# Performance work log

Hardware: AMD Instinct MI355X
Metric: run time of the kernel (lower is better)

The kernel has to match this reference:

```python
import jax, jax.numpy as jnp
import numpy as np

# Segmented tensor-product configuration (matches init_kwargs)
NUM_SEG = 32   # segments per operand
MUL = 128      # multiplicity ('u' axis) of operand0 / output segments
D = 3          # irrep dimension (2l+1 with l=1) for i, j, k axes
NUM_PATHS = 64
BATCH = 2048


def setup_inputs() -> dict:
    key = jax.random.key(0)
    k0, k1, k2, k3, k4, k5 = jax.random.split(key, 6)
    x0 = jax.random.normal(k0, (BATCH, NUM_SEG * MUL * D), dtype=jnp.float32)
    x1 = jax.random.normal(k1, (BATCH, NUM_SEG * D), dtype=jnp.float32)
    coeff = jax.random.normal(k2, (NUM_PATHS, D, D, D), dtype=jnp.float32)
    idx0 = jax.random.randint(k3, (NUM_PATHS,), 0, NUM_SEG, dtype=jnp.int32)
    idx1 = jax.random.randint(k4, (NUM_PATHS,), 0, NUM_SEG, dtype=jnp.int32)
    idx2 = jax.random.randint(k5, (NUM_PATHS,), 0, NUM_SEG, dtype=jnp.int32)
    return {"x0": x0, "x1": x1, "coeff": coeff,
            "idx0": idx0, "idx1": idx1, "idx2": idx2}


def reference(x0, x1, coeff, idx0, idx1, idx2):
    # Segmented CG tensor product:
    #   out[seg2][u,k] += sum_{paths p with idx2[p]==seg2}
    #       sum_ij x0[idx0[p]][u,i] * x1[idx1[p]][j] * coeff[p][i,j,k]
    B = x0.shape[0]
    x0s = x0.reshape(B, NUM_SEG, MUL, D)   # 'ui' segments
    x1s = x1.reshape(B, NUM_SEG, D)        # 'j' segments
    # gather input segments per path
    x0p = x0s[:, idx0]                     # (B, P, MUL, D)
    x1p = x1s[:, idx1]                     # (B, P, D)
    # per-path contraction with path coefficients, path axis first for scatter
    contrib = jnp.einsum('bpui,bpj,pijk->pbuk', x0p, x1p, coeff)
    # scatter-add contributions into output segments
    out_seg = jax.ops.segment_sum(contrib, idx2, num_segments=NUM_SEG)  # (S, B, MUL, D)
    out = jnp.transpose(out_seg, (1, 0, 2, 3)).reshape(B, NUM_SEG * MUL * D)
    return out
```

## Files before the change

kernel.cpp:

```cpp
#include <hip/hip_runtime.h>

#define NUM_SEG 32
#define MUL 128
#define D 3
#define NUM_PATHS 64
#define ROW (NUM_SEG * MUL * D)
#define SEGF (MUL * D)
#define HALF_F4 1536
#define SEG_HF 192

typedef float v2f __attribute__((ext_vector_type(2)));
typedef float v4f __attribute__((ext_vector_type(4)));

__global__ __launch_bounds__(256) void ftp_kernel(
    const float* __restrict__ x0, const float* __restrict__ x1,
    const float* __restrict__ coeff, const int* __restrict__ idx0,
    const int* __restrict__ idx1, const int* __restrict__ idx2,
    float* __restrict__ out)
{
    const int bid = blockIdx.x;
    const int b   = bid >> 1;
    const int h   = bid & 1;
    const int tid = threadIdx.x;

    __shared__ v4f   s_x0[HALF_F4];
    __shared__ float s_m[NUM_PATHS][9];
    __shared__ unsigned short s_pe[NUM_SEG][NUM_PATHS];
    __shared__ int   s_cnt[NUM_SEG];

    if (tid < NUM_SEG) s_cnt[tid] = 0;
    __syncthreads();

    const v4f* __restrict__ src = (const v4f*)(x0 + (size_t)b * ROW);
    #pragma unroll
    for (int j = 0; j < 6; ++j) {
        const int f     = j * 256 + tid;
        const int seg   = f / 48;
        const int inner = f - seg * 48;
        s_x0[f] = src[seg * 96 + h * 48 + inner];
    }

    if (tid < NUM_PATHS) {
        const int p  = tid;
        const int s0 = idx0[p];
        const int i1 = idx1[p];
        const int s2 = idx2[p];
        const int pos = atomicAdd(&s_cnt[s2], 1);
        s_pe[s2][pos] = (unsigned short)(s0 | (p << 8));

        const float* xr = x1 + (size_t)b * (NUM_SEG * D) + i1 * D;
        const float j0 = xr[0], j1 = xr[1], j2 = xr[2];
        const float* cf = coeff + p * 27;
        #pragma unroll
        for (int i = 0; i < D; ++i)
            #pragma unroll
            for (int k = 0; k < D; ++k)
                s_m[p][i * 3 + k] = j0 * cf[i * 9 + k]
                                  + j1 * cf[i * 9 + 3 + k]
                                  + j2 * cf[i * 9 + 6 + k];
    }
    __syncthreads();

    const int q  = tid & 31;
    const int ss = tid >> 5;
    float* __restrict__ ob = out + (size_t)b * ROW + h * SEG_HF + q * 6;
    const float* __restrict__ sx = (const float*)s_x0;

    #pragma unroll
    for (int si = 0; si < 4; ++si) {
        const int s = ss + si * 8;
        float a00 = 0, a01 = 0, a02 = 0, a10 = 0, a11 = 0, a12 = 0;
        const int n = s_cnt[s];
        for (int t = 0; t < n; ++t) {
            const int e = s_pe[s][t];
            const float* xs = sx + (e & 255) * SEG_HF + q * 6;
            const float u00 = xs[0], u01 = xs[1], u02 = xs[2];
            const float u10 = xs[3], u11 = xs[4], u12 = xs[5];
            const float* m = s_m[e >> 8];
            a00 += u00 * m[0] + u01 * m[3] + u02 * m[6];
            a01 += u00 * m[1] + u01 * m[4] + u02 * m[7];
            a02 += u00 * m[2] + u01 * m[5] + u02 * m[8];
            a10 += u10 * m[0] + u11 * m[3] + u12 * m[6];
            a11 += u10 * m[1] + u11 * m[4] + u12 * m[7];
            a12 += u10 * m[2] + u11 * m[5] + u12 * m[8];
        }
        float* o = ob + s * SEGF;
        v2f O0 = {a00, a01}, O1 = {a02, a10}, O2 = {a11, a12};
        *(v2f*)(o + 0) = O0;
        *(v2f*)(o + 2) = O1;
        *(v2f*)(o + 4) = O2;
    }
}

extern "C" void kernel_launch(void* const* d_in, const int* in_sizes, int n_in,
                              void* d_out, int out_size, void* d_ws, size_t ws_size,
                              hipStream_t stream) {
    const float* x0    = (const float*)d_in[0];
    const float* x1    = (const float*)d_in[1];
    const float* coeff = (const float*)d_in[2];
    const int*   idx0  = (const int*)d_in[3];
    const int*   idx1  = (const int*)d_in[4];
    const int*   idx2  = (const int*)d_in[5];
    float* out = (float*)d_out;

    const int B = in_sizes[0] / ROW;
    ftp_kernel<<<B * 2, 256, 0, stream>>>(x0, x1, coeff, idx0, idx1, idx2, out);
}
```

Measured before the change: 192.1 us.

## Split into setup and main kernels reading x0 directly from global memory

Adds a setup kernel that builds the per-segment path schedule once and precomputes the per-batch, per-path 3x3 contracted matrices into workspace. The main kernel then skips LDS staging of x0 and reads segments straight from global memory with 128-bit vector loads, each thread handling four u-rows and two output segments. The aim is to remove the per-block LDS fill, the syncthreads and the redundant schedule building. The cost is an extra kernel launch, a global round trip for the matrices, and repeated uncached gathers of x0 segments when several paths share the same source segment. The original kernel remains as a fallback when the workspace is too small.

```diff
diff --git a/kernel.cpp b/kernel.cpp
--- a/kernel.cpp
+++ b/kernel.cpp
@@ -6,11 +6,119 @@
 #define NUM_PATHS 64
 #define ROW (NUM_SEG * MUL * D)
 #define SEGF (MUL * D)
-#define HALF_F4 1536
 #define SEG_HF 192
+#define PE_STRIDE 64
+#define M_PAD 12
 
 typedef float v2f __attribute__((ext_vector_type(2)));
 typedef float v4f __attribute__((ext_vector_type(4)));
+
+__global__ __launch_bounds__(64) void ftp_setup(
+    const float* __restrict__ x1, const float* __restrict__ coeff,
+    const int* __restrict__ idx0, const int* __restrict__ idx1,
+    const int* __restrict__ idx2,
+    unsigned int* __restrict__ sched, float* __restrict__ m)
+{
+    const int tid = threadIdx.x;
+    if (blockIdx.x == 0) {
+        __shared__ int lcnt[NUM_SEG];
+        __shared__ unsigned int lpe[NUM_SEG][PE_STRIDE];
+        if (tid < NUM_SEG) lcnt[tid] = 0;
+        __syncthreads();
+        {
+            const int p   = tid;
+            const int s2  = idx2[p];
+            const int pos = atomicAdd(&lcnt[s2], 1);
+            lpe[s2][pos]  = (unsigned int)(idx0[p] | (p << 8));
+        }
+        __syncthreads();
+        if (tid < NUM_SEG) sched[tid] = (unsigned int)lcnt[tid];
+        for (int j = tid; j < NUM_SEG * PE_STRIDE; j += 64) {
+            const int s = j / PE_STRIDE, t = j % PE_STRIDE;
+            sched[NUM_SEG + j] = (t < lcnt[s]) ? lpe[s][t] : 0u;
+        }
+    } else {
+        const int b = blockIdx.x - 1;
+        const int p = tid;
+        const float* xr = x1 + (size_t)b * (NUM_SEG * D) + idx1[p] * D;
+        const float j0 = xr[0], j1 = xr[1], j2 = xr[2];
+        const float* cf = coeff + p * 27;
+        float mv[M_PAD];
+        #pragma unroll
+        for (int i = 0; i < D; ++i)
+            #pragma unroll
+            for (int k = 0; k < D; ++k)
+                mv[i * 3 + k] = j0 * cf[i * 9 + k]
+                              + j1 * cf[i * 9 + 3 + k]
+                              + j2 * cf[i * 9 + 6 + k];
+        mv[9] = 0.f; mv[10] = 0.f; mv[11] = 0.f;
+        float* mp = m + ((size_t)b * NUM_PATHS + p) * M_PAD;
+        *(v4f*)(mp)     = *(const v4f*)(mv);
+        *(v4f*)(mp + 4) = *(const v4f*)(mv + 4);
+        *(v4f*)(mp + 8) = *(const v4f*)(mv + 8);
+    }
+}
+
+__global__ __launch_bounds__(256) void ftp_main(
+    const float* __restrict__ x0, const unsigned int* __restrict__ sched,
+    const float* __restrict__ m, float* __restrict__ out)
+{
+    const int bid = blockIdx.x;
+    const int b   = bid >> 1;
+    const int h   = bid & 1;
+    const int tid = threadIdx.x;
+    const int qq  = tid & 15;
+    const int ss  = tid >> 4;
+
+    const float* __restrict__ xb = x0  + (size_t)b * ROW + h * SEG_HF + qq * 12;
+    float* __restrict__       ob = out + (size_t)b * ROW + h * SEG_HF + qq * 12;
+    const float* __restrict__ mb = m + (size_t)b * NUM_PATHS * M_PAD;
+    const unsigned int* __restrict__ pe = sched + NUM_SEG;
+
+    const int n0 = (int)sched[ss];
+    const int n1 = (int)sched[ss + 16];
+
+    #pragma unroll
+    for (int si = 0; si < 2; ++si) {
+        const int s = ss + si * 16;
+        const int n = si ? n1 : n0;
+        const unsigned int* __restrict__ pes = pe + s * PE_STRIDE;
+        float a00 = 0, a01 = 0, a02 = 0, a10 = 0, a11 = 0, a12 = 0;
+        float a20 = 0, a21 = 0, a22 = 0, a30 = 0, a31 = 0, a32 = 0;
+        for (int t = 0; t < n; ++t) {
+            const unsigned e = pes[t];
+            const float* xs = xb + (e & 255u) * SEGF;
+            const v4f X0 = *(const v4f*)(xs);
+            const v4f X1 = *(const v4f*)(xs + 4);
+            const v4f X2 = *(const v4f*)(xs + 8);
+            const float* mp = mb + (e >> 8) * M_PAD;
+            const v4f MA = *(const v4f*)(mp);
+            const v4f MB = *(const v4f*)(mp + 4);
+            const float m22 = mp[8];
+            a00 += X0.x * MA.x + X0.y * MA.w + X0.z * MB.z;
+            a01 += X0.x * MA.y + X0.y * MB.x + X0.z * MB.w;
+            a02 += X0.x * MA.z + X0.y * MB.y + X0.z * m22;
+            a10 += X0.w * MA.x + X1.x * MA.w + X1.y * MB.z;
+            a11 += X0.w * MA.y + X1.x * MB.x + X1.y * MB.w;
+            a12 += X0.w * MA.z + X1.x * MB.y + X1.y * m22;
+            a20 += X1.z * MA.x + X1.w * MA.w + X2.x * MB.z;
+            a21 += X1.z * MA.y + X1.w * MB.x + X2.x * MB.w;
+            a22 += X1.z * MA.z + X1.w * MB.y + X2.x * m22;
+            a30 += X2.y * MA.x + X2.z * MA.w + X2.w * MB.z;
+            a31 += X2.y * MA.y + X2.z * MB.x + X2.w * MB.w;
+            a32 += X2.y * MA.z + X2.z * MB.y + X2.w * m22;
+        }
+        float* o = ob + s * SEGF;
+        v4f O0 = {a00, a01, a02, a10};
+        v4f O1 = {a11, a12, a20, a21};
+        v4f O2 = {a22, a30, a31, a32};
+        *(v4f*)(o)     = O0;
+        *(v4f*)(o + 4) = O1;
+        *(v4f*)(o + 8) = O2;
+    }
+}
+
+#define HALF_F4 1536
 
 __global__ __launch_bounds__(256) void ftp_kernel(
     const float* __restrict__ x0, const float* __restrict__ x1,
@@ -76,13 +184,13 @@
             const float* xs = sx + (e & 255) * SEG_HF + q * 6;
             const float u00 = xs[0], u01 = xs[1], u02 = xs[2];
             const float u10 = xs[3], u11 = xs[4], u12 = xs[5];
-            const float* m = s_m[e >> 8];
-            a00 += u00 * m[0] + u01 * m[3] + u02 * m[6];
-            a01 += u00 * m[1] + u01 * m[4] + u02 * m[7];
-            a02 += u00 * m[2] + u01 * m[5] + u02 * m[8];
-            a10 += u10 * m[0] + u11 * m[3] + u12 * m[6];
-            a11 += u10 * m[1] + u11 * m[4] + u12 * m[7];
-            a12 += u10 * m[2] + u11 * m[5] + u12 * m[8];
+            const float* mm = s_m[e >> 8];
+            a00 += u00 * mm[0] + u01 * mm[3] + u02 * mm[6];
+            a01 += u00 * mm[1] + u01 * mm[4] + u02 * mm[7];
+            a02 += u00 * mm[2] + u01 * mm[5] + u02 * mm[8];
+            a10 += u10 * mm[0] + u11 * mm[3] + u12 * mm[6];
+            a11 += u10 * mm[1] + u11 * mm[4] + u12 * mm[7];
+            a12 += u10 * mm[2] + u11 * mm[5] + u12 * mm[8];
         }
         float* o = ob + s * SEGF;
         v2f O0 = {a00, a01}, O1 = {a02, a10}, O2 = {a11, a12};
@@ -104,5 +212,17 @@
     float* out = (float*)d_out;
 
     const int B = in_sizes[0] / ROW;
-    ftp_kernel<<<B * 2, 256, 0, stream>>>(x0, x1, coeff, idx0, idx1, idx2, out);
-}
+
+    const size_t schedBytes = (size_t)(NUM_SEG + NUM_SEG * PE_STRIDE) * sizeof(unsigned int);
+    const size_t schedPad   = (schedBytes + 255) & ~(size_t)255;
+    const size_t mBytes     = (size_t)B * NUM_PATHS * M_PAD * sizeof(float);
+
+    if (ws_size >= schedPad + mBytes) {
+        unsigned int* sched = (unsigned int*)d_ws;
+        float*        m     = (float*)((char*)d_ws + schedPad);
+        ftp_setup<<<B + 1, 64, 0, stream>>>(x1, coeff, idx0, idx1, idx2, sched, m);
+        ftp_main<<<B * 2, 256, 0, stream>>>(x0, sched, m, out);
+    } else {
+        ftp_kernel<<<B * 2, 256, 0, stream>>>(x0, x1, coeff, idx0, idx1, idx2, out);
+    }
+}
```

New measurement: 214.9 us. +11.9%, slower.

## Process full batch row per block with direct-to-LDS loads and sorted segment schedule

Applied to the files above, without the earlier changes.

Each block now handles a whole batch row instead of half of one. The full 48KB x0 row is staged into LDS with global_load_lds, so data goes straight to shared memory without passing through registers. Path entries are compacted with prefix offsets, and output segments are sorted by path count and dealt to waves in a snake order to balance the work. Block indices are swizzled across groups of eight. The larger LDS footprint lowers the number of resident blocks per CU, and the serial insertion sort on one thread adds a small setup cost.

```diff
diff --git a/kernel.cpp b/kernel.cpp
--- a/kernel.cpp
+++ b/kernel.cpp
@@ -6,8 +6,6 @@
 #define NUM_PATHS 64
 #define ROW (NUM_SEG * MUL * D)
 #define SEGF (MUL * D)
-#define HALF_F4 1536
-#define SEG_HF 192
 
 typedef float v2f __attribute__((ext_vector_type(2)));
 typedef float v4f __attribute__((ext_vector_type(4)));
@@ -16,73 +14,102 @@
     const float* __restrict__ x0, const float* __restrict__ x1,
     const float* __restrict__ coeff, const int* __restrict__ idx0,
     const int* __restrict__ idx1, const int* __restrict__ idx2,
-    float* __restrict__ out)
+    float* __restrict__ out, int swz)
 {
     const int bid = blockIdx.x;
-    const int b   = bid >> 1;
-    const int h   = bid & 1;
+    const int nb  = gridDim.x;
+    const int b   = swz ? ((bid & 7) * (nb >> 3) + (bid >> 3)) : bid;
     const int tid = threadIdx.x;
 
-    __shared__ v4f   s_x0[HALF_F4];
-    __shared__ float s_m[NUM_PATHS][9];
-    __shared__ unsigned short s_pe[NUM_SEG][NUM_PATHS];
-    __shared__ int   s_cnt[NUM_SEG];
-
-    if (tid < NUM_SEG) s_cnt[tid] = 0;
-    __syncthreads();
+    __shared__ __align__(16) float s_x0[ROW];
+    __shared__ __align__(16) float s_m[NUM_PATHS][9];
+    __shared__ int s_cnt[NUM_SEG];
+    __shared__ int s_off[NUM_SEG];
+    __shared__ int s_perm[NUM_SEG];
+    __shared__ unsigned int s_sched[NUM_SEG];
+    __shared__ unsigned short s_ent[NUM_PATHS];
 
     const v4f* __restrict__ src = (const v4f*)(x0 + (size_t)b * ROW);
     #pragma unroll
-    for (int j = 0; j < 6; ++j) {
-        const int f     = j * 256 + tid;
-        const int seg   = f / 48;
-        const int inner = f - seg * 48;
-        s_x0[f] = src[seg * 96 + h * 48 + inner];
+    for (int j = 0; j < 12; ++j) {
+        const int F = j * 256 + tid;
+        __builtin_amdgcn_global_load_lds(
+            (const __attribute__((address_space(1))) void*)(src + F),
+            (__attribute__((address_space(3))) void*)((v4f*)s_x0 + F),
+            16, 0, 0);
     }
+
+    if (tid < NUM_SEG) s_cnt[tid] = 0;
+    asm volatile("s_waitcnt lgkmcnt(0)" ::: "memory");
+    __builtin_amdgcn_s_barrier();
 
     if (tid < NUM_PATHS) {
         const int p  = tid;
+        const int s2 = idx2[p];
         const int s0 = idx0[p];
-        const int i1 = idx1[p];
-        const int s2 = idx2[p];
-        const int pos = atomicAdd(&s_cnt[s2], 1);
-        s_pe[s2][pos] = (unsigned short)(s0 | (p << 8));
-
-        const float* xr = x1 + (size_t)b * (NUM_SEG * D) + i1 * D;
+        const float* xr = x1 + (size_t)b * (NUM_SEG * D) + idx1[p] * D;
         const float j0 = xr[0], j1 = xr[1], j2 = xr[2];
         const float* cf = coeff + p * 27;
+        float mv[9];
         #pragma unroll
         for (int i = 0; i < D; ++i)
             #pragma unroll
             for (int k = 0; k < D; ++k)
-                s_m[p][i * 3 + k] = j0 * cf[i * 9 + k]
-                                  + j1 * cf[i * 9 + 3 + k]
-                                  + j2 * cf[i * 9 + 6 + k];
+                mv[i * 3 + k] = j0 * cf[i * 9 + k]
+                              + j1 * cf[i * 9 + 3 + k]
+                              + j2 * cf[i * 9 + 6 + k];
+
+        const int pos = atomicAdd(&s_cnt[s2], 1);
+        if (tid == 0) {
+            int off = 0;
+            #pragma unroll
+            for (int s = 0; s < NUM_SEG; ++s) { s_off[s] = off; off += s_cnt[s]; }
+            int perm[NUM_SEG];
+            for (int s = 0; s < NUM_SEG; ++s) perm[s] = s;
+            for (int i = 1; i < NUM_SEG; ++i) {
+                int v = perm[i], cv = s_cnt[v], j = i - 1;
+                while (j >= 0 && s_cnt[perm[j]] < cv) { perm[j + 1] = perm[j]; --j; }
+                perm[j + 1] = v;
+            }
+            for (int s = 0; s < NUM_SEG; ++s) s_perm[s] = perm[s];
+        }
+        s_ent[s_off[s2] + pos] = (unsigned short)(s0 | (p << 8));
+        if (tid < NUM_SEG) {
+            const int sg = s_perm[tid];
+            s_sched[tid] = (unsigned)s_cnt[sg] | ((unsigned)s_off[sg] << 8)
+                         | ((unsigned)sg << 16);
+        }
+        #pragma unroll
+        for (int i = 0; i < 9; ++i) s_m[p][i] = mv[i];
     }
-    __syncthreads();
 
-    const int q  = tid & 31;
-    const int ss = tid >> 5;
-    float* __restrict__ ob = out + (size_t)b * ROW + h * SEG_HF + q * 6;
-    const float* __restrict__ sx = (const float*)s_x0;
+    asm volatile("s_waitcnt vmcnt(0) lgkmcnt(0)" ::: "memory");
+    __builtin_amdgcn_s_barrier();
+
+    const int q = tid & 63;
+    const int w = tid >> 6;
+    float* __restrict__ ob = out + (size_t)b * ROW + q * 6;
 
     #pragma unroll
-    for (int si = 0; si < 4; ++si) {
-        const int s = ss + si * 8;
+    for (int si = 0; si < 8; ++si) {
+        const int rank = si * 4 + ((si & 1) ? (3 - w) : w);
+        const unsigned sc = s_sched[rank];
+        const int n   = sc & 255;
+        const int off = (sc >> 8) & 255;
+        const int s   = sc >> 16;
         float a00 = 0, a01 = 0, a02 = 0, a10 = 0, a11 = 0, a12 = 0;
-        const int n = s_cnt[s];
         for (int t = 0; t < n; ++t) {
-            const int e = s_pe[s][t];
-            const float* xs = sx + (e & 255) * SEG_HF + q * 6;
+            const int e = s_ent[off + t];
+            const float* xs = s_x0 + (e & 255) * SEGF + q * 6;
             const float u00 = xs[0], u01 = xs[1], u02 = xs[2];
             const float u10 = xs[3], u11 = xs[4], u12 = xs[5];
-            const float* m = s_m[e >> 8];
-            a00 += u00 * m[0] + u01 * m[3] + u02 * m[6];
-            a01 += u00 * m[1] + u01 * m[4] + u02 * m[7];
-            a02 += u00 * m[2] + u01 * m[5] + u02 * m[8];
-            a10 += u10 * m[0] + u11 * m[3] + u12 * m[6];
-            a11 += u10 * m[1] + u11 * m[4] + u12 * m[7];
-            a12 += u10 * m[2] + u11 * m[5] + u12 * m[8];
+            const float* mm = s_m[e >> 8];
+            a00 += u00 * mm[0] + u01 * mm[3] + u02 * mm[6];
+            a01 += u00 * mm[1] + u01 * mm[4] + u02 * mm[7];
+            a02 += u00 * mm[2] + u01 * mm[5] + u02 * mm[8];
+            a10 += u10 * mm[0] + u11 * mm[3] + u12 * mm[6];
+            a11 += u10 * mm[1] + u11 * mm[4] + u12 * mm[7];
+            a12 += u10 * mm[2] + u11 * mm[5] + u12 * mm[8];
         }
         float* o = ob + s * SEGF;
         v2f O0 = {a00, a01}, O1 = {a02, a10}, O2 = {a11, a12};
@@ -104,5 +131,6 @@
     float* out = (float*)d_out;
 
     const int B = in_sizes[0] / ROW;
-    ftp_kernel<<<B * 2, 256, 0, stream>>>(x0, x1, coeff, idx0, idx1, idx2, out);
+    const int swz = (B % 8 == 0) ? 1 : 0;
+    ftp_kernel<<<B, 256, 0, stream>>>(x0, x1, coeff, idx0, idx1, idx2, out, swz);
 }
```

New measurement: 233.8 us. 21.7% more time.
